# Kernel tuning notes

Hardware: AMD Instinct MI355X
Metric: run time of the kernel (lower is better)

Reference implementation:

```python
import jax, jax.numpy as jnp
import numpy as np

H = 256          # hidden_size
HH, WW = 4, 4
CONV = HH * WW * H   # 4096, conv_out_size
N = 16           # n_subtasks
S = 32           # subtask_size
B = 256          # batch
T = 128          # timesteps
TOT = N + S + H + S + 1 + 1  # 338, RecurrentState width


def setup_inputs() -> dict:
    key = jax.random.key(0)
    ks = jax.random.split(key, 12)
    w = lambda k, shape: (jax.random.normal(k, shape) * 0.02).astype(jnp.float32)
    obs = jax.random.normal(ks[0], (T, B, CONV), jnp.float32)
    task = jax.random.normal(ks[1], (B, N, S), jnp.float32)
    hx0 = jnp.zeros((B, TOT), jnp.float32).at[:, :N].set(1.0 / N)  # uniform pointer init
    return dict(
        obs=obs, task=task, hx0=hx0,
        W_ih=w(ks[2], (3 * H, H)), W_hh=w(ks[3], (3 * H, H)),
        b_ih=jnp.zeros((3 * H,), jnp.float32), b_hh=jnp.zeros((3 * H,), jnp.float32),
        W_f=w(ks[4], (H, CONV + 2 * S + 1)), b_f=jnp.zeros((H,), jnp.float32),
        W_u=w(ks[5], (1, 2 * H)), b_u=jnp.zeros((1,), jnp.float32),
        W_s=w(ks[6], (3, H)), b_s=jnp.zeros((3,), jnp.float32),
        W_pi=w(ks[7], (N, H + S)), b_pi=jnp.zeros((N,), jnp.float32),
        W_beta=w(ks[8], (2, CONV + S)), b_beta=jnp.zeros((2,), jnp.float32),
    )


def reference(obs, task, hx0, W_ih, W_hh, b_ih, b_hh, W_f, b_f, W_u, b_u,
              W_s, b_s, W_pi, b_pi, W_beta, b_beta):
    M = task  # [B, N, S] subtask memory
    p0 = hx0[:, :N]
    r0 = hx0[:, N:N + S]
    h0 = hx0[:, N + S:N + S + H]
    g0 = hx0[:, N + S + H:N + S + H + S]
    b0 = hx0[:, N + S + H + S:N + S + H + S + 1]
    keys = jax.random.split(jax.random.key(42), T * 2).reshape(T, 2)

    def gru(x, h):  # torch.nn.GRUCell math
        gi = x @ W_ih.T + b_ih
        gh = h @ W_hh.T + b_hh
        ir, iz, inn = jnp.split(gi, 3, axis=-1)
        hr, hz, hn = jnp.split(gh, 3, axis=-1)
        rr = jax.nn.sigmoid(ir + hr)
        z = jax.nn.sigmoid(iz + hz)
        n = jnp.tanh(inn + rr * hn)
        return (1.0 - z) * n + z * h

    def step(carry, xs):
        p, r, h, b = carry[0], carry[1], carry[2], carry[4]
        g = carry[3]
        x, kk = xs
        # s = f(cat(x, r, g, b))
        s = jnp.concatenate([x, r, g, b], axis=-1) @ W_f.T + b_f
        # update gate c = sigmoid(phi_update(cat(s, h)))
        c = jax.nn.sigmoid(jnp.concatenate([s, h], axis=-1) @ W_u.T + b_u)  # [B,1]
        h_new = gru(s, h)
        # pointer shift: l = softmax(phi_shift(h_old)); p = conv1d(p, l) (same-pad, k=3)
        l = jax.nn.softmax(h @ W_s.T + b_s, axis=1)  # [B,3]
        pp = jnp.pad(p, ((0, 0), (1, 1)))
        p_new = l[:, 0:1] * pp[:, :N] + l[:, 1:2] * pp[:, 1:N + 1] + l[:, 2:3] * pp[:, 2:N + 2]
        # memory read r = p @ M
        r_new = jnp.einsum('bn,bns->bs', p_new, M)
        p = c * p_new + (1.0 - c) * p
        r = c * r_new + (1.0 - c) * r
        h = c * h_new + (1.0 - c) * h
        # sample g ~ Cat(pi_theta(h, r)); g embedding = selected memory row
        logits_g = jnp.concatenate([h, r], axis=-1) @ W_pi.T + b_pi  # [B,N]
        g_idx = jax.random.categorical(kk[0], logits_g)  # [B] int
        lp_g = jnp.take_along_axis(jax.nn.log_softmax(logits_g, axis=-1), g_idx[:, None], axis=1)  # [B,1]
        g_vec = jnp.take_along_axis(M, g_idx[:, None, None], axis=1)[:, 0, :]  # [B,S]
        g = c * g_vec + (1.0 - c) * g
        # sample b ~ Cat(beta(x, g))
        logits_b = jnp.concatenate([x, g], axis=-1) @ W_beta.T + b_beta  # [B,2]
        b_idx = jax.random.categorical(kk[1], logits_b)
        lp_b = jnp.take_along_axis(jax.nn.log_softmax(logits_b, axis=-1), b_idx[:, None], axis=1)
        b = b_idx[:, None].astype(jnp.float32)
        log_prob = lp_g + lp_b
        out = jnp.concatenate([p, r, h, g, b, log_prob], axis=-1)  # [B, TOT]
        return (p, r, h, g, b), out

    _, outs = jax.lax.scan(step, (p0, r0, h0, g0, b0), (obs, keys))
    return outs  # [T, B, TOT]
```

## Files before the change

kernel.cpp:

```cpp
#include <hip/hip_runtime.h>


#define RNG_PARTITIONABLE 1

#define T_STEPS 128
#define B_ROWS  256
#define TOT     338
#define CONV    4096
#define LDWF    4161
#define LDWB    4128

__device__ __forceinline__ void tf2x32(unsigned k0, unsigned k1, unsigned c0, unsigned c1,
                                       unsigned &o0, unsigned &o1) {
  const unsigned ks2 = k0 ^ k1 ^ 0x1BD11BDAu;
  unsigned x0 = c0 + k0;
  unsigned x1 = c1 + k1;
#define TFR(r) { x0 += x1; x1 = (x1 << (r)) | (x1 >> (32 - (r))); x1 ^= x0; }
  TFR(13) TFR(15) TFR(26) TFR(6)
  x0 += k1; x1 += ks2 + 1u;
  TFR(17) TFR(29) TFR(16) TFR(24)
  x0 += ks2; x1 += k0 + 2u;
  TFR(13) TFR(15) TFR(26) TFR(6)
  x0 += k0; x1 += k1 + 3u;
  TFR(17) TFR(29) TFR(16) TFR(24)
  x0 += k1; x1 += ks2 + 4u;
  TFR(13) TFR(15) TFR(26) TFR(6)
  x0 += ks2; x1 += k0 + 5u;
#undef TFR
  o0 = x0; o1 = x1;
}

__device__ __forceinline__ void rng_key(unsigned j, unsigned &k0, unsigned &k1) {
#if RNG_PARTITIONABLE
  tf2x32(0u, 42u, 0u, j, k0, k1);
#else
  unsigned w[2];
  for (int q = 0; q < 2; ++q) {
    unsigned i = 2u*j + (unsigned)q, a, b;
    if (i < 256u) { tf2x32(0u, 42u, i, 256u + i, a, b); w[q] = a; }
    else          { tf2x32(0u, 42u, i - 256u, i, a, b); w[q] = b; }
  }
  k0 = w[0]; k1 = w[1];
#endif
}

__device__ __forceinline__ unsigned rng_bits(unsigned k0, unsigned k1, unsigned idx, unsigned total) {
#if RNG_PARTITIONABLE
  unsigned o0, o1;
  tf2x32(k0, k1, 0u, idx, o0, o1);
  return o0 ^ o1;
#else
  unsigned half = total >> 1, o0, o1;
  if (idx < half) { tf2x32(k0, k1, idx, half + idx, o0, o1); return o0; }
  else            { tf2x32(k0, k1, idx - half, idx, o0, o1); return o1; }
#endif
}

__device__ __forceinline__ float gumbel_from_bits(unsigned bits) {
  float u0 = __uint_as_float(0x3f800000u | (bits >> 9)) - 1.0f;
  float u  = fmaxf(u0, 1.17549435e-38f);
  return -logf(-logf(u));
}

__global__ __launch_bounds__(256) void rng_k(float* __restrict__ ggum, float* __restrict__ bgum) {
  unsigned tid = blockIdx.x * 256u + threadIdx.x;
  const unsigned NG = T_STEPS * B_ROWS * 16;
  const unsigned NB = T_STEPS * B_ROWS * 2;
  if (tid < NG) {
    unsigned t = tid / (B_ROWS * 16);
    unsigned i = tid % (B_ROWS * 16);
    unsigned k0, k1; rng_key(2u * t, k0, k1);
    ggum[tid] = gumbel_from_bits(rng_bits(k0, k1, i, B_ROWS * 16));
  } else if (tid < NG + NB) {
    unsigned q = tid - NG;
    unsigned t = q / (B_ROWS * 2);
    unsigned i = q % (B_ROWS * 2);
    unsigned k0, k1; rng_key(2u * t + 1u, k0, k1);
    bgum[q] = gumbel_from_bits(rng_bits(k0, k1, i, B_ROWS * 2));
  }
}

__global__ __launch_bounds__(256) void prep_k(const float* __restrict__ W_ih,
                                              const float* __restrict__ W_hh,
                                              const float* __restrict__ W_f,
                                              const float* __restrict__ W_pi,
                                              float* __restrict__ WihT, float* __restrict__ WhhT,
                                              float* __restrict__ WfT, float* __restrict__ wpiT) {
  int tid = blockIdx.x * 256 + threadIdx.x;
  const int NW = 768 * 256;
  if (tid < NW) {
    int k = tid / 768, rem = tid % 768;
    WihT[tid] = W_ih[rem * 256 + k];
    WhhT[tid] = W_hh[rem * 256 + k];
  } else if (tid < NW + 65 * 256) {
    int q = tid - NW; int j = q >> 8, o = q & 255;
    WfT[q] = W_f[(size_t)o * LDWF + CONV + j];
  } else if (tid < NW + 65 * 256 + 288 * 16) {
    int q = tid - NW - 65 * 256; int kk = q / 16, o = q % 16;
    wpiT[q] = W_pi[o * 288 + kk];
  }
}

__device__ __forceinline__ float waveRed(float v) {
  v += __shfl_down(v, 32, 64);
  v += __shfl_down(v, 16, 64);
  v += __shfl_down(v, 8, 64);
  v += __shfl_down(v, 4, 64);
  v += __shfl_down(v, 2, 64);
  v += __shfl_down(v, 1, 64);
  return v;
}

__global__ __launch_bounds__(256) void bx_k(const float* __restrict__ obs,
                                            const float* __restrict__ W_beta,
                                            const float* __restrict__ b_beta,
                                            float* __restrict__ bxv) {
  int m = blockIdx.x, tid = threadIdx.x;
  const float* row = obs + (size_t)m * CONV;
  float p0 = 0.f, p1 = 0.f;
  for (int i = tid; i < CONV; i += 256) {
    float o = row[i];
    p0 = fmaf(o, W_beta[i], p0);
    p1 = fmaf(o, W_beta[LDWB + i], p1);
  }
  p0 = waveRed(p0); p1 = waveRed(p1);
  __shared__ float sc[2][4];
  int w = tid >> 6;
  if ((tid & 63) == 0) { sc[0][w] = p0; sc[1][w] = p1; }
  __syncthreads();
  if (tid == 0) bxv[(size_t)m * 2 + 0] = sc[0][0] + sc[0][1] + sc[0][2] + sc[0][3] + b_beta[0];
  if (tid == 1) bxv[(size_t)m * 2 + 1] = sc[1][0] + sc[1][1] + sc[1][2] + sc[1][3] + b_beta[1];
}

struct __attribute__((packed, aligned(4))) F4 { float x, y, z, w; };

__global__ __launch_bounds__(256) void gemm1_k(const float* __restrict__ A,
                                               const float* __restrict__ W,
                                               const float* __restrict__ bias,
                                               float* __restrict__ C1) {
  __shared__ __align__(16) float As[32][68];
  __shared__ __align__(16) float Bs[32][68];
  int bid = blockIdx.x;
  int mt = bid & 511, nt = bid >> 9;
  int m0 = mt * 64, n0 = nt * 64;
  int tid = threadIdx.x;
  int tm = tid & 15, tn = tid >> 4;
  int lr = tid >> 2;
  int lc = (tid & 3) * 8;
  float acc[4][4] = {};
  for (int k0 = 0; k0 < CONV; k0 += 32) {
    F4 a0 = *(const F4*)(A + (size_t)(m0 + lr) * CONV + k0 + lc);
    F4 a1 = *(const F4*)(A + (size_t)(m0 + lr) * CONV + k0 + lc + 4);
    F4 b0 = *(const F4*)(W + (size_t)(n0 + lr) * LDWF + k0 + lc);
    F4 b1 = *(const F4*)(W + (size_t)(n0 + lr) * LDWF + k0 + lc + 4);
    __syncthreads();
    As[lc + 0][lr] = a0.x; As[lc + 1][lr] = a0.y; As[lc + 2][lr] = a0.z; As[lc + 3][lr] = a0.w;
    As[lc + 4][lr] = a1.x; As[lc + 5][lr] = a1.y; As[lc + 6][lr] = a1.z; As[lc + 7][lr] = a1.w;
    Bs[lc + 0][lr] = b0.x; Bs[lc + 1][lr] = b0.y; Bs[lc + 2][lr] = b0.z; Bs[lc + 3][lr] = b0.w;
    Bs[lc + 4][lr] = b1.x; Bs[lc + 5][lr] = b1.y; Bs[lc + 6][lr] = b1.z; Bs[lc + 7][lr] = b1.w;
    __syncthreads();
#pragma unroll
    for (int kk = 0; kk < 32; ++kk) {
      const float4 av = *(const float4*)&As[kk][tm * 4];
      const float4 bv = *(const float4*)&Bs[kk][tn * 4];
      acc[0][0] = fmaf(av.x, bv.x, acc[0][0]); acc[0][1] = fmaf(av.x, bv.y, acc[0][1]);
      acc[0][2] = fmaf(av.x, bv.z, acc[0][2]); acc[0][3] = fmaf(av.x, bv.w, acc[0][3]);
      acc[1][0] = fmaf(av.y, bv.x, acc[1][0]); acc[1][1] = fmaf(av.y, bv.y, acc[1][1]);
      acc[1][2] = fmaf(av.y, bv.z, acc[1][2]); acc[1][3] = fmaf(av.y, bv.w, acc[1][3]);
      acc[2][0] = fmaf(av.z, bv.x, acc[2][0]); acc[2][1] = fmaf(av.z, bv.y, acc[2][1]);
      acc[2][2] = fmaf(av.z, bv.z, acc[2][2]); acc[2][3] = fmaf(av.z, bv.w, acc[2][3]);
      acc[3][0] = fmaf(av.w, bv.x, acc[3][0]); acc[3][1] = fmaf(av.w, bv.y, acc[3][1]);
      acc[3][2] = fmaf(av.w, bv.z, acc[3][2]); acc[3][3] = fmaf(av.w, bv.w, acc[3][3]);
    }
  }
  const int mrow = m0 + tm * 4;
  const int ncol = n0 + tn * 4;
  float4 bv4 = *(const float4*)(bias + ncol);
#pragma unroll
  for (int i = 0; i < 4; ++i) {
    float4 v;
    v.x = acc[i][0] + bv4.x; v.y = acc[i][1] + bv4.y;
    v.z = acc[i][2] + bv4.z; v.w = acc[i][3] + bv4.w;
    *(float4*)(C1 + (size_t)(mrow + i) * 256 + ncol) = v;
  }
}

__global__ __launch_bounds__(256, 1) void seq_k(
    const float* __restrict__ hx0, const float* __restrict__ task,
    const float* __restrict__ WfT, const float* __restrict__ WihT,
    const float* __restrict__ WhhT, const float* __restrict__ b_ih,
    const float* __restrict__ b_hh, const float* __restrict__ W_u,
    const float* __restrict__ b_u, const float* __restrict__ W_s,
    const float* __restrict__ b_s, const float* __restrict__ b_pi,
    const float* __restrict__ W_beta, const float* __restrict__ C1,
    const float* __restrict__ bxv, const float* __restrict__ wpiT,
    const float* __restrict__ ggum, const float* __restrict__ bgum,
    float* __restrict__ out) {
  const int b = blockIdx.x;
  const int tid = threadIdx.x;

  __shared__ float h_sh[256], s_sh[256], M_sh[512];
  __shared__ float p_sh[16], pn_sh[16], r_sh[32], g_sh[32];
  __shared__ float red4[4][4];
  __shared__ float red16[4][16];
  __shared__ float logit_sh[16];
  __shared__ float l_sh[3];
  __shared__ float c_sh, b_sh;
  __shared__ int gidx_sh;
  __shared__ float misc_sh[3];

  h_sh[tid] = hx0[b * TOT + 48 + tid];
  if (tid < 16) p_sh[tid] = hx0[b * TOT + tid];
  if (tid < 32) {
    r_sh[tid] = hx0[b * TOT + 16 + tid];
    g_sh[tid] = hx0[b * TOT + 304 + tid];
  }
  if (tid == 0) b_sh = hx0[b * TOT + 336];
  M_sh[tid]       = task[(size_t)b * 512 + tid];
  M_sh[256 + tid] = task[(size_t)b * 512 + 256 + tid];

  const float bih_r = b_ih[tid], bih_z = b_ih[256 + tid], bih_n = b_ih[512 + tid];
  const float bhh_r = b_hh[tid], bhh_z = b_hh[256 + tid], bhh_n = b_hh[512 + tid];
  const float wu_s = W_u[tid], wu_h = W_u[256 + tid];
  const float ws0 = W_s[tid], ws1 = W_s[256 + tid], ws2 = W_s[512 + tid];
  const float bu0 = b_u[0], bs0 = b_s[0], bs1 = b_s[1], bs2 = b_s[2];
  __syncthreads();

  for (int t = 0; t < T_STEPS; ++t) {
    float sacc = C1[((size_t)t * 256 + b) * 256 + tid];
#pragma unroll
    for (int j = 0; j < 32; ++j) sacc = fmaf(r_sh[j], WfT[j * 256 + tid], sacc);
#pragma unroll
    for (int j = 0; j < 32; ++j) sacc = fmaf(g_sh[j], WfT[(32 + j) * 256 + tid], sacc);
    sacc = fmaf(b_sh, WfT[64 * 256 + tid], sacc);
    s_sh[tid] = sacc;
    __syncthreads();

    float gi_r = 0.f, gi_z = 0.f, gi_n = 0.f;
    float gh_r = 0.f, gh_z = 0.f, gh_n = 0.f;
#pragma unroll 8
    for (int k = 0; k < 256; ++k) {
      const float sv = s_sh[k];
      const float hv = h_sh[k];
      const float* wi = WihT + k * 768 + tid;
      const float* wh = WhhT + k * 768 + tid;
      gi_r = fmaf(sv, wi[0],   gi_r);
      gi_z = fmaf(sv, wi[256], gi_z);
      gi_n = fmaf(sv, wi[512], gi_n);
      gh_r = fmaf(hv, wh[0],   gh_r);
      gh_z = fmaf(hv, wh[256], gh_z);
      gh_n = fmaf(hv, wh[512], gh_n);
    }
    const float hold = h_sh[tid];
    {
      float pc = fmaf(wu_s, sacc, wu_h * hold);
      float p0 = ws0 * hold, p1 = ws1 * hold, p2 = ws2 * hold;
      pc = waveRed(pc); p0 = waveRed(p0); p1 = waveRed(p1); p2 = waveRed(p2);
      int w = tid >> 6;
      if ((tid & 63) == 0) { red4[w][0] = pc; red4[w][1] = p0; red4[w][2] = p1; red4[w][3] = p2; }
    }
    __syncthreads();
    if (tid == 0) {
      float cs = red4[0][0] + red4[1][0] + red4[2][0] + red4[3][0] + bu0;
      c_sh = 1.0f / (1.0f + expf(-cs));
      float x0 = red4[0][1] + red4[1][1] + red4[2][1] + red4[3][1] + bs0;
      float x1 = red4[0][2] + red4[1][2] + red4[2][2] + red4[3][2] + bs1;
      float x2 = red4[0][3] + red4[1][3] + red4[2][3] + red4[3][3] + bs2;
      float m = fmaxf(x0, fmaxf(x1, x2));
      float e0 = expf(x0 - m), e1 = expf(x1 - m), e2 = expf(x2 - m);
      float es = e0 + e1 + e2;
      l_sh[0] = e0 / es; l_sh[1] = e1 / es; l_sh[2] = e2 / es;
    }
    __syncthreads();
    const float c = c_sh, omc = 1.0f - c;

    float hg;
    {
      float rr = 1.0f / (1.0f + expf(-(gi_r + bih_r + gh_r + bhh_r)));
      float zz = 1.0f / (1.0f + expf(-(gi_z + bih_z + gh_z + bhh_z)));
      float nn = tanhf(gi_n + bih_n + rr * (gh_n + bhh_n));
      float hnew = (1.0f - zz) * nn + zz * hold;
      hg = c * hnew + omc * hold;
      h_sh[tid] = hg;
    }
    if (tid < 16) {
      float pm1 = (tid > 0) ? p_sh[tid - 1] : 0.f;
      float pp1 = (tid < 15) ? p_sh[tid + 1] : 0.f;
      pn_sh[tid] = l_sh[0] * pm1 + l_sh[1] * p_sh[tid] + l_sh[2] * pp1;
    }
    __syncthreads();
    float rv = 0.f;
    if (tid < 32) {
      float acc = 0.f;
#pragma unroll
      for (int n2 = 0; n2 < 16; ++n2) acc = fmaf(pn_sh[n2], M_sh[n2 * 32 + tid], acc);
      rv = c * acc + omc * r_sh[tid];
      r_sh[tid] = rv;
    }
    if (tid < 16) p_sh[tid] = c * pn_sh[tid] + omc * p_sh[tid];

    {
      float part[16];
      const float* wrow = wpiT + tid * 16;
#pragma unroll
      for (int o = 0; o < 16; ++o) part[o] = hg * wrow[o];
      if (tid < 32) {
        const float* wrow2 = wpiT + (256 + tid) * 16;
#pragma unroll
        for (int o = 0; o < 16; ++o) part[o] = fmaf(rv, wrow2[o], part[o]);
      }
#pragma unroll
      for (int o = 0; o < 16; ++o) part[o] = waveRed(part[o]);
      int w = tid >> 6;
      if ((tid & 63) == 0) {
#pragma unroll
        for (int o = 0; o < 16; ++o) red16[w][o] = part[o];
      }
    }
    __syncthreads();
    if (tid < 16)
      logit_sh[tid] = red16[0][tid] + red16[1][tid] + red16[2][tid] + red16[3][tid] + b_pi[tid];
    __syncthreads();
    if (tid == 0) {
      const float* gg = ggum + ((size_t)t * 256 + b) * 16;
      float best = -3.402823466e+38f; int gidx = 0;
      for (int n2 = 0; n2 < 16; ++n2) {
        float v = logit_sh[n2] + gg[n2];
        if (v > best) { best = v; gidx = n2; }
      }
      float mx = logit_sh[0];
      for (int n2 = 1; n2 < 16; ++n2) mx = fmaxf(mx, logit_sh[n2]);
      float se = 0.f;
      for (int n2 = 0; n2 < 16; ++n2) se += expf(logit_sh[n2] - mx);
      misc_sh[0] = logit_sh[gidx] - mx - logf(se);
      gidx_sh = gidx;
    }
    __syncthreads();
    if (tid < 32) g_sh[tid] = c * M_sh[gidx_sh * 32 + tid] + omc * g_sh[tid];
    __syncthreads();
    if (tid == 0) {
      const float* bx2 = bxv + ((size_t)t * 256 + b) * 2;
      float lb0 = bx2[0], lb1 = bx2[1];
      for (int s2 = 0; s2 < 32; ++s2) {
        float gv = g_sh[s2];
        lb0 = fmaf(gv, W_beta[CONV + s2], lb0);
        lb1 = fmaf(gv, W_beta[LDWB + CONV + s2], lb1);
      }
      const float* bg = bgum + ((size_t)t * 256 + b) * 2;
      int bidx = ((lb1 + bg[1]) > (lb0 + bg[0])) ? 1 : 0;
      float mb = fmaxf(lb0, lb1);
      float seb = expf(lb0 - mb) + expf(lb1 - mb);
      float lpb = (bidx ? lb1 : lb0) - mb - logf(seb);
      misc_sh[1] = (float)bidx;
      misc_sh[2] = misc_sh[0] + lpb;
      b_sh = (float)bidx;
    }
    __syncthreads();
    {
      size_t base = ((size_t)t * 256 + b) * TOT;
      float v;
      if (tid < 16) v = p_sh[tid];
      else if (tid < 48) v = r_sh[tid - 16];
      else v = h_sh[tid - 48];
      out[base + tid] = v;
      if (tid < 82) {
        int s2 = tid + 256;
        float v2;
        if (s2 < 304) v2 = h_sh[s2 - 48];
        else if (s2 < 336) v2 = g_sh[s2 - 304];
        else if (s2 == 336) v2 = misc_sh[1];
        else v2 = misc_sh[2];
        out[base + s2] = v2;
      }
    }
    __syncthreads();
  }
}

extern "C" void kernel_launch(void* const* d_in, const int* in_sizes, int n_in,
                              void* d_out, int out_size, void* d_ws, size_t ws_size,
                              hipStream_t stream) {
  const float* obs    = (const float*)d_in[0];
  const float* task   = (const float*)d_in[1];
  const float* hx0    = (const float*)d_in[2];
  const float* W_ih   = (const float*)d_in[3];
  const float* W_hh   = (const float*)d_in[4];
  const float* b_ih   = (const float*)d_in[5];
  const float* b_hh   = (const float*)d_in[6];
  const float* W_f    = (const float*)d_in[7];
  const float* b_f    = (const float*)d_in[8];
  const float* W_u    = (const float*)d_in[9];
  const float* b_u    = (const float*)d_in[10];
  const float* W_s    = (const float*)d_in[11];
  const float* b_s    = (const float*)d_in[12];
  const float* W_pi   = (const float*)d_in[13];
  const float* b_pi   = (const float*)d_in[14];
  const float* W_beta = (const float*)d_in[15];
  const float* b_beta = (const float*)d_in[16];

  char* ws = (char*)d_ws;
  size_t off = 0;
  auto take = [&](size_t bytes) {
    size_t r = off;
    off += (bytes + 255) & ~(size_t)255;
    return r;
  };
  size_t off_wpiT = take((size_t)288 * 16 * 4);
  size_t off_WihT = take((size_t)768 * 256 * 4);
  size_t off_WhhT = take((size_t)768 * 256 * 4);
  size_t off_WfT  = take((size_t)65 * 256 * 4);
  size_t off_ggum = take((size_t)T_STEPS * B_ROWS * 16 * 4);
  size_t off_bgum = take((size_t)T_STEPS * B_ROWS * 2 * 4);
  size_t off_bx   = take((size_t)T_STEPS * B_ROWS * 2 * 4);
  size_t off_C1   = take((size_t)T_STEPS * B_ROWS * 256 * 4);
  if (off > ws_size) return;

  float* wpiT = (float*)(ws + off_wpiT);
  float* WihT = (float*)(ws + off_WihT);
  float* WhhT = (float*)(ws + off_WhhT);
  float* WfT  = (float*)(ws + off_WfT);
  float* ggum = (float*)(ws + off_ggum);
  float* bgum = (float*)(ws + off_bgum);
  float* bxv  = (float*)(ws + off_bx);
  float* C1   = (float*)(ws + off_C1);

  hipLaunchKernelGGL(prep_k, dim3(851), dim3(256), 0, stream, W_ih, W_hh, W_f, W_pi,
                     WihT, WhhT, WfT, wpiT);
  hipLaunchKernelGGL(rng_k, dim3(2304), dim3(256), 0, stream, ggum, bgum);
  hipLaunchKernelGGL(gemm1_k, dim3(2048), dim3(256), 0, stream, obs, W_f, b_f, C1);
  hipLaunchKernelGGL(bx_k, dim3(32768), dim3(256), 0, stream, obs, W_beta, b_beta, bxv);
  hipLaunchKernelGGL(seq_k, dim3(256), dim3(256), 0, stream,
                     hx0, task, WfT, WihT, WhhT, b_ih, b_hh, W_u, b_u, W_s, b_s, b_pi,
                     W_beta, C1, bxv, wpiT, ggum, bgum, (float*)d_out);
}
```

Measured before the change: 3.864 ms.

## Widen sequential GRU kernel to 768 threads with interleaved weights and LDS-cached params

```diff
diff --git a/kernel.cpp b/kernel.cpp
--- a/kernel.cpp
+++ b/kernel.cpp
@@ -80,25 +80,13 @@
   }
 }
 
-__global__ __launch_bounds__(256) void prep_k(const float* __restrict__ W_ih,
-                                              const float* __restrict__ W_hh,
-                                              const float* __restrict__ W_f,
-                                              const float* __restrict__ W_pi,
-                                              float* __restrict__ WihT, float* __restrict__ WhhT,
-                                              float* __restrict__ WfT, float* __restrict__ wpiT) {
-  int tid = blockIdx.x * 256 + threadIdx.x;
-  const int NW = 768 * 256;
-  if (tid < NW) {
-    int k = tid / 768, rem = tid % 768;
-    WihT[tid] = W_ih[rem * 256 + k];
-    WhhT[tid] = W_hh[rem * 256 + k];
-  } else if (tid < NW + 65 * 256) {
-    int q = tid - NW; int j = q >> 8, o = q & 255;
-    WfT[q] = W_f[(size_t)o * LDWF + CONV + j];
-  } else if (tid < NW + 65 * 256 + 288 * 16) {
-    int q = tid - NW - 65 * 256; int kk = q / 16, o = q % 16;
-    wpiT[q] = W_pi[o * 288 + kk];
-  }
+__global__ __launch_bounds__(256) void prep2_k(const float* __restrict__ W_ih,
+                                               const float* __restrict__ W_hh,
+                                               float2* __restrict__ WT2) {
+  int col = blockIdx.x;
+  int k = threadIdx.x;
+  WT2[(size_t)k * 768 + col] =
+      make_float2(W_ih[(size_t)col * 256 + k], W_hh[(size_t)col * 256 + k]);
 }
 
 __device__ __forceinline__ float waveRed(float v) {
@@ -185,21 +173,27 @@
   }
 }
 
-__global__ __launch_bounds__(256, 1) void seq_k(
+__global__ __launch_bounds__(768, 1) void seq_k(
     const float* __restrict__ hx0, const float* __restrict__ task,
-    const float* __restrict__ WfT, const float* __restrict__ WihT,
-    const float* __restrict__ WhhT, const float* __restrict__ b_ih,
-    const float* __restrict__ b_hh, const float* __restrict__ W_u,
-    const float* __restrict__ b_u, const float* __restrict__ W_s,
-    const float* __restrict__ b_s, const float* __restrict__ b_pi,
+    const float* __restrict__ W_f, const float* __restrict__ WT2,
+    const float* __restrict__ b_ih, const float* __restrict__ b_hh,
+    const float* __restrict__ W_u, const float* __restrict__ b_u,
+    const float* __restrict__ W_s, const float* __restrict__ b_s,
+    const float* __restrict__ W_pi, const float* __restrict__ b_pi,
     const float* __restrict__ W_beta, const float* __restrict__ C1,
-    const float* __restrict__ bxv, const float* __restrict__ wpiT,
-    const float* __restrict__ ggum, const float* __restrict__ bgum,
-    float* __restrict__ out) {
+    const float* __restrict__ bxv, const float* __restrict__ ggum,
+    const float* __restrict__ bgum, float* __restrict__ out) {
   const int b = blockIdx.x;
   const int tid = threadIdx.x;
-
-  __shared__ float h_sh[256], s_sh[256], M_sh[512];
+  const int o = tid & 255;
+  const int part = tid >> 8;
+  const float2* __restrict__ WT2v = (const float2*)WT2;
+
+  __shared__ float wf_sh[65 * 256];
+  __shared__ float wpi_sh[288 * 16];
+  __shared__ float2 shb[256];
+  __shared__ float2 gsum[2][256];
+  __shared__ float M_sh[512];
   __shared__ float p_sh[16], pn_sh[16], r_sh[32], g_sh[32];
   __shared__ float red4[4][4];
   __shared__ float red16[4][16];
@@ -208,56 +202,77 @@
   __shared__ float c_sh, b_sh;
   __shared__ int gidx_sh;
   __shared__ float misc_sh[3];
-
-  h_sh[tid] = hx0[b * TOT + 48 + tid];
+  __shared__ float gg_sh[16], bg_sh[2], bx_sh[2];
+  __shared__ float wb_sh[2][32], bpi_sh[16];
+
+  for (int i = tid; i < 65 * 256; i += 768) {
+    int oo = i / 65, j = i % 65;
+    wf_sh[i] = W_f[(size_t)oo * LDWF + CONV + j];
+  }
+  for (int i = tid; i < 288 * 16; i += 768) wpi_sh[i] = W_pi[i];
+  if (part == 0) shb[o] = make_float2(0.f, hx0[b * TOT + 48 + o]);
   if (tid < 16) p_sh[tid] = hx0[b * TOT + tid];
   if (tid < 32) {
     r_sh[tid] = hx0[b * TOT + 16 + tid];
     g_sh[tid] = hx0[b * TOT + 304 + tid];
-  }
+    wb_sh[0][tid] = W_beta[CONV + tid];
+    wb_sh[1][tid] = W_beta[LDWB + CONV + tid];
+  }
+  if (tid >= 32 && tid < 48) bpi_sh[tid - 32] = b_pi[tid - 32];
   if (tid == 0) b_sh = hx0[b * TOT + 336];
-  M_sh[tid]       = task[(size_t)b * 512 + tid];
-  M_sh[256 + tid] = task[(size_t)b * 512 + 256 + tid];
-
-  const float bih_r = b_ih[tid], bih_z = b_ih[256 + tid], bih_n = b_ih[512 + tid];
-  const float bhh_r = b_hh[tid], bhh_z = b_hh[256 + tid], bhh_n = b_hh[512 + tid];
-  const float wu_s = W_u[tid], wu_h = W_u[256 + tid];
-  const float ws0 = W_s[tid], ws1 = W_s[256 + tid], ws2 = W_s[512 + tid];
+  if (tid < 512) M_sh[tid] = task[(size_t)b * 512 + tid];
+
+  const float bih_r = b_ih[o], bih_z = b_ih[256 + o], bih_n = b_ih[512 + o];
+  const float bhh_r = b_hh[o], bhh_z = b_hh[256 + o], bhh_n = b_hh[512 + o];
+  const float wu_s = W_u[o], wu_h = W_u[256 + o];
+  const float ws0 = W_s[o], ws1 = W_s[256 + o], ws2 = W_s[512 + o];
   const float bu0 = b_u[0], bs0 = b_s[0], bs1 = b_s[1], bs2 = b_s[2];
   __syncthreads();
 
+  float c1v = (part == 0) ? C1[(size_t)b * 256 + o] : 0.f;
+  float sacc = 0.f, hold = 0.f;
+
   for (int t = 0; t < T_STEPS; ++t) {
-    float sacc = C1[((size_t)t * 256 + b) * 256 + tid];
-#pragma unroll
-    for (int j = 0; j < 32; ++j) sacc = fmaf(r_sh[j], WfT[j * 256 + tid], sacc);
-#pragma unroll
-    for (int j = 0; j < 32; ++j) sacc = fmaf(g_sh[j], WfT[(32 + j) * 256 + tid], sacc);
-    sacc = fmaf(b_sh, WfT[64 * 256 + tid], sacc);
-    s_sh[tid] = sacc;
-    __syncthreads();
-
-    float gi_r = 0.f, gi_z = 0.f, gi_n = 0.f;
-    float gh_r = 0.f, gh_z = 0.f, gh_n = 0.f;
+    if (part == 0) {
+      hold = shb[o].y;
+      sacc = c1v;
+      const float* wfr = wf_sh + o * 65;
+#pragma unroll
+      for (int j = 0; j < 32; ++j) sacc = fmaf(r_sh[j], wfr[j], sacc);
+#pragma unroll
+      for (int j = 0; j < 32; ++j) sacc = fmaf(g_sh[j], wfr[32 + j], sacc);
+      sacc = fmaf(b_sh, wfr[64], sacc);
+      shb[o].x = sacc;
+    }
+    __syncthreads();
+
+    if (part == 0) {
+      int tn2 = (t + 1 < T_STEPS) ? t + 1 : t;
+      c1v = C1[((size_t)tn2 * 256 + b) * 256 + o];
+    } else if (tid < 272) {
+      gg_sh[tid - 256] = ggum[((size_t)t * 256 + b) * 16 + (tid - 256)];
+    } else if (tid < 274) {
+      bg_sh[tid - 272] = bgum[((size_t)t * 256 + b) * 2 + (tid - 272)];
+    } else if (tid < 276) {
+      bx_sh[tid - 274] = bxv[((size_t)t * 256 + b) * 2 + (tid - 274)];
+    }
+
+    float ai = 0.f, ah = 0.f;
 #pragma unroll 8
     for (int k = 0; k < 256; ++k) {
-      const float sv = s_sh[k];
-      const float hv = h_sh[k];
-      const float* wi = WihT + k * 768 + tid;
-      const float* wh = WhhT + k * 768 + tid;
-      gi_r = fmaf(sv, wi[0],   gi_r);
-      gi_z = fmaf(sv, wi[256], gi_z);
-      gi_n = fmaf(sv, wi[512], gi_n);
-      gh_r = fmaf(hv, wh[0],   gh_r);
-      gh_z = fmaf(hv, wh[256], gh_z);
-      gh_n = fmaf(hv, wh[512], gh_n);
-    }
-    const float hold = h_sh[tid];
-    {
+      float2 w = WT2v[(size_t)k * 768 + tid];
+      float2 sh2 = shb[k];
+      ai = fmaf(sh2.x, w.x, ai);
+      ah = fmaf(sh2.y, w.y, ah);
+    }
+    if (part == 0) {
       float pc = fmaf(wu_s, sacc, wu_h * hold);
-      float p0 = ws0 * hold, p1 = ws1 * hold, p2 = ws2 * hold;
-      pc = waveRed(pc); p0 = waveRed(p0); p1 = waveRed(p1); p2 = waveRed(p2);
-      int w = tid >> 6;
-      if ((tid & 63) == 0) { red4[w][0] = pc; red4[w][1] = p0; red4[w][2] = p1; red4[w][3] = p2; }
+      float q0 = ws0 * hold, q1 = ws1 * hold, q2 = ws2 * hold;
+      pc = waveRed(pc); q0 = waveRed(q0); q1 = waveRed(q1); q2 = waveRed(q2);
+      int w4 = tid >> 6;
+      if ((tid & 63) == 0) { red4[w4][0] = pc; red4[w4][1] = q0; red4[w4][2] = q1; red4[w4][3] = q2; }
+    } else {
+      gsum[part - 1][o] = make_float2(ai, ah);
     }
     __syncthreads();
     if (tid == 0) {
@@ -273,15 +288,16 @@
     }
     __syncthreads();
     const float c = c_sh, omc = 1.0f - c;
-
-    float hg;
-    {
-      float rr = 1.0f / (1.0f + expf(-(gi_r + bih_r + gh_r + bhh_r)));
-      float zz = 1.0f / (1.0f + expf(-(gi_z + bih_z + gh_z + bhh_z)));
-      float nn = tanhf(gi_n + bih_n + rr * (gh_n + bhh_n));
+    float hg = 0.f;
+    if (part == 0) {
+      float2 gz = gsum[0][o];
+      float2 gn = gsum[1][o];
+      float rr = 1.0f / (1.0f + expf(-(ai + bih_r + ah + bhh_r)));
+      float zz = 1.0f / (1.0f + expf(-(gz.x + bih_z + gz.y + bhh_z)));
+      float nn = tanhf(gn.x + bih_n + rr * (gn.y + bhh_n));
       float hnew = (1.0f - zz) * nn + zz * hold;
       hg = c * hnew + omc * hold;
-      h_sh[tid] = hg;
+      shb[o].y = hg;
     }
     if (tid < 16) {
       float pm1 = (tid > 0) ? p_sh[tid - 1] : 0.f;
@@ -298,34 +314,30 @@
       r_sh[tid] = rv;
     }
     if (tid < 16) p_sh[tid] = c * pn_sh[tid] + omc * p_sh[tid];
-
-    {
-      float part[16];
-      const float* wrow = wpiT + tid * 16;
-#pragma unroll
-      for (int o = 0; o < 16; ++o) part[o] = hg * wrow[o];
+    if (part == 0) {
+      float pv[16];
+#pragma unroll
+      for (int o2 = 0; o2 < 16; ++o2) pv[o2] = hg * wpi_sh[o2 * 288 + tid];
       if (tid < 32) {
-        const float* wrow2 = wpiT + (256 + tid) * 16;
-#pragma unroll
-        for (int o = 0; o < 16; ++o) part[o] = fmaf(rv, wrow2[o], part[o]);
+#pragma unroll
+        for (int o2 = 0; o2 < 16; ++o2) pv[o2] = fmaf(rv, wpi_sh[o2 * 288 + 256 + tid], pv[o2]);
       }
 #pragma unroll
-      for (int o = 0; o < 16; ++o) part[o] = waveRed(part[o]);
-      int w = tid >> 6;
+      for (int o2 = 0; o2 < 16; ++o2) pv[o2] = waveRed(pv[o2]);
+      int w4 = tid >> 6;
       if ((tid & 63) == 0) {
 #pragma unroll
-        for (int o = 0; o < 16; ++o) red16[w][o] = part[o];
+        for (int o2 = 0; o2 < 16; ++o2) red16[w4][o2] = pv[o2];
       }
     }
     __syncthreads();
     if (tid < 16)
-      logit_sh[tid] = red16[0][tid] + red16[1][tid] + red16[2][tid] + red16[3][tid] + b_pi[tid];
+      logit_sh[tid] = red16[0][tid] + red16[1][tid] + red16[2][tid] + red16[3][tid] + bpi_sh[tid];
     __syncthreads();
     if (tid == 0) {
-      const float* gg = ggum + ((size_t)t * 256 + b) * 16;
       float best = -3.402823466e+38f; int gidx = 0;
       for (int n2 = 0; n2 < 16; ++n2) {
-        float v = logit_sh[n2] + gg[n2];
+        float v = logit_sh[n2] + gg_sh[n2];
         if (v > best) { best = v; gidx = n2; }
       }
       float mx = logit_sh[0];
@@ -339,15 +351,13 @@
     if (tid < 32) g_sh[tid] = c * M_sh[gidx_sh * 32 + tid] + omc * g_sh[tid];
     __syncthreads();
     if (tid == 0) {
-      const float* bx2 = bxv + ((size_t)t * 256 + b) * 2;
-      float lb0 = bx2[0], lb1 = bx2[1];
+      float lb0 = bx_sh[0], lb1 = bx_sh[1];
       for (int s2 = 0; s2 < 32; ++s2) {
         float gv = g_sh[s2];
-        lb0 = fmaf(gv, W_beta[CONV + s2], lb0);
-        lb1 = fmaf(gv, W_beta[LDWB + CONV + s2], lb1);
+        lb0 = fmaf(gv, wb_sh[0][s2], lb0);
+        lb1 = fmaf(gv, wb_sh[1][s2], lb1);
       }
-      const float* bg = bgum + ((size_t)t * 256 + b) * 2;
-      int bidx = ((lb1 + bg[1]) > (lb0 + bg[0])) ? 1 : 0;
+      int bidx = ((lb1 + bg_sh[1]) > (lb0 + bg_sh[0])) ? 1 : 0;
       float mb = fmaxf(lb0, lb1);
       float seb = expf(lb0 - mb) + expf(lb1 - mb);
       float lpb = (bidx ? lb1 : lb0) - mb - logf(seb);
@@ -356,22 +366,16 @@
       b_sh = (float)bidx;
     }
     __syncthreads();
-    {
+    if (tid < TOT) {
       size_t base = ((size_t)t * 256 + b) * TOT;
       float v;
       if (tid < 16) v = p_sh[tid];
       else if (tid < 48) v = r_sh[tid - 16];
-      else v = h_sh[tid - 48];
+      else if (tid < 304) v = shb[tid - 48].y;
+      else if (tid < 336) v = g_sh[tid - 304];
+      else if (tid == 336) v = misc_sh[1];
+      else v = misc_sh[2];
       out[base + tid] = v;
-      if (tid < 82) {
-        int s2 = tid + 256;
-        float v2;
-        if (s2 < 304) v2 = h_sh[s2 - 48];
-        else if (s2 < 336) v2 = g_sh[s2 - 304];
-        else if (s2 == 336) v2 = misc_sh[1];
-        else v2 = misc_sh[2];
-        out[base + s2] = v2;
-      }
     }
     __syncthreads();
   }
@@ -405,31 +409,24 @@
     off += (bytes + 255) & ~(size_t)255;
     return r;
   };
-  size_t off_wpiT = take((size_t)288 * 16 * 4);
-  size_t off_WihT = take((size_t)768 * 256 * 4);
-  size_t off_WhhT = take((size_t)768 * 256 * 4);
-  size_t off_WfT  = take((size_t)65 * 256 * 4);
+  size_t off_WT2  = take((size_t)768 * 256 * 8);
   size_t off_ggum = take((size_t)T_STEPS * B_ROWS * 16 * 4);
   size_t off_bgum = take((size_t)T_STEPS * B_ROWS * 2 * 4);
   size_t off_bx   = take((size_t)T_STEPS * B_ROWS * 2 * 4);
   size_t off_C1   = take((size_t)T_STEPS * B_ROWS * 256 * 4);
   if (off > ws_size) return;
 
-  float* wpiT = (float*)(ws + off_wpiT);
-  float* WihT = (float*)(ws + off_WihT);
-  float* WhhT = (float*)(ws + off_WhhT);
-  float* WfT  = (float*)(ws + off_WfT);
+  float* WT2  = (float*)(ws + off_WT2);
   float* ggum = (float*)(ws + off_ggum);
   float* bgum = (float*)(ws + off_bgum);
   float* bxv  = (float*)(ws + off_bx);
   float* C1   = (float*)(ws + off_C1);
 
-  hipLaunchKernelGGL(prep_k, dim3(851), dim3(256), 0, stream, W_ih, W_hh, W_f, W_pi,
-                     WihT, WhhT, WfT, wpiT);
+  hipLaunchKernelGGL(prep2_k, dim3(768), dim3(256), 0, stream, W_ih, W_hh, (float2*)WT2);
   hipLaunchKernelGGL(rng_k, dim3(2304), dim3(256), 0, stream, ggum, bgum);
   hipLaunchKernelGGL(gemm1_k, dim3(2048), dim3(256), 0, stream, obs, W_f, b_f, C1);
   hipLaunchKernelGGL(bx_k, dim3(32768), dim3(256), 0, stream, obs, W_beta, b_beta, bxv);
-  hipLaunchKernelGGL(seq_k, dim3(256), dim3(256), 0, stream,
-                     hx0, task, WfT, WihT, WhhT, b_ih, b_hh, W_u, b_u, W_s, b_s, b_pi,
-                     W_beta, C1, bxv, wpiT, ggum, bgum, (float*)d_out);
-}
+  hipLaunchKernelGGL(seq_k, dim3(256), dim3(768), 0, stream,
+                     hx0, task, W_f, WT2, b_ih, b_hh, W_u, b_u, W_s, b_s, W_pi, b_pi,
+                     W_beta, C1, bxv, ggum, bgum, (float*)d_out);
+}
```

After: 4.590 ms. 18.8% more time.
